# Optimization experiments

Measured on AMD Instinct MI355X. Metric: run time of the kernel, lower is better.

Reference implementation:

```python
import jax, jax.numpy as jnp
import numpy as np

N_MB = 4  # number of micro-behavior buckets; C = N_MB**2 + 1

def setup_inputs() -> dict:
    key = jax.random.key(0)
    k_q, k_k, k_b, k_w, k_a = jax.random.split(key, 5)
    b, h, S, d = 8, 8, 512, 64
    C = N_MB * N_MB + 1
    return {
        "query": jax.random.normal(k_q, (b, h, S, d), dtype=jnp.float32),
        "key": jax.random.normal(k_k, (b, h, S, d), dtype=jnp.float32),
        "b_seq": jax.random.randint(k_b, (b, S), 0, N_MB + 1, dtype=jnp.int32),
        "W1": jax.random.normal(k_w, (N_MB, h, d, d), dtype=jnp.float32) * 0.02,
        "alpha1": jax.random.normal(k_a, (C, N_MB, h), dtype=jnp.float32) * 0.02,
    }

def reference(query, key, b_seq, W1, alpha1):
    # bucket-pair index per (i, j) token pair; 0 if either token is padding
    bi = b_seq[:, :, None]  # [b, S, 1]
    bj = b_seq[:, None, :]  # [b, 1, S]
    b_mat = ((bi - 1) * N_MB + bj) * (bi * bj != 0).astype(jnp.int32)  # [b, S, S]
    # mix the n_mb base bilinear weights into C per-bucket-pair matrices
    W1_ = jnp.einsum('Bhmn,CBh->Chmn', W1, jax.nn.softmax(alpha1, axis=1))
    # full bilinear score for every bucket-pair class C (the wasteful part)
    att_all = jnp.einsum('bhim,Chmn,bhjn->bhijC', query, W1_, key)  # [b,h,S,S,C]
    # select the score matching each pair's bucket index
    idx = b_mat[:, None, :, :, None].astype(jnp.int32)  # [b,1,S,S,1] -> broadcast over h
    idx = jnp.broadcast_to(idx, att_all.shape[:4] + (1,))
    scores = jnp.take_along_axis(att_all, idx, axis=4)[..., 0]  # [b,h,S,S]
    return scores
```

## Files before the change

kernel.cpp:

```cpp
#include <hip/hip_runtime.h>
#include <stdint.h>

#define NB 4
#define NC 17
#define HH 8
#define SS 512
#define DD 64
#define CT 64

typedef __attribute__((ext_vector_type(8))) short bf16x8;
typedef __attribute__((ext_vector_type(4))) float f32x4;

#define WS_W1   0
#define WS_RIDX 1114112
#define WS_GST  (WS_RIDX + 16384)

__device__ __forceinline__ unsigned short f2bf(float f) {
  unsigned int x; __builtin_memcpy(&x, &f, 4);
  return (unsigned short)((x + 0x7fff + ((x >> 16) & 1)) >> 16);
}
__device__ __forceinline__ bf16x8 cvt8(float4 a, float4 b) {
  union { bf16x8 v; unsigned short u[8]; } t;
  t.u[0] = f2bf(a.x); t.u[1] = f2bf(a.y); t.u[2] = f2bf(a.z); t.u[3] = f2bf(a.w);
  t.u[4] = f2bf(b.x); t.u[5] = f2bf(b.y); t.u[6] = f2bf(b.z); t.u[7] = f2bf(b.w);
  return t.v;
}

__global__ __launch_bounds__(256) void k_prep(const int* __restrict__ bseq,
                                              const float* __restrict__ W1,
                                              const float* __restrict__ alpha,
                                              int* __restrict__ ridx,
                                              int* __restrict__ gst,
                                              unsigned short* __restrict__ W1mbf) {
  int tid = threadIdx.x;
  if (blockIdx.x < 8) {
    int b = blockIdx.x;
    __shared__ int cnt[5], base[6], cur[5];
    if (tid < 5) cnt[tid] = 0;
    __syncthreads();
    for (int j = tid; j < SS; j += blockDim.x) atomicAdd(&cnt[bseq[b * SS + j]], 1);
    __syncthreads();
    if (tid == 0) {
      base[0] = 0;
      for (int k = 0; k < 5; k++) base[k + 1] = base[k] + cnt[k];
      for (int k = 0; k < 6; k++) gst[b * 6 + k] = base[k];
    }
    __syncthreads();
    if (tid < 5) cur[tid] = base[tid];
    __syncthreads();
    for (int j = tid; j < SS; j += blockDim.x) {
      int p = atomicAdd(&cur[bseq[b * SS + j]], 1);
      ridx[b * SS + p] = j;
    }
  } else {
    int cb = blockIdx.x - 8;
    int c = cb >> 3, hh = cb & 7;
    __shared__ float sm[NB];
    if (tid == 0) {
      float a[NB], mx = -1e30f;
      for (int B = 0; B < NB; B++) { a[B] = alpha[(c * NB + B) * HH + hh]; mx = fmaxf(mx, a[B]); }
      float s = 0.f;
      for (int B = 0; B < NB; B++) { a[B] = __expf(a[B] - mx); s += a[B]; }
      for (int B = 0; B < NB; B++) sm[B] = a[B] / s;
    }
    __syncthreads();
    float s0 = sm[0], s1 = sm[1], s2 = sm[2], s3 = sm[3];
    for (int idx = tid; idx < DD * DD; idx += blockDim.x) {
      float v = W1[((0 * HH + hh) * DD * DD) + idx] * s0 +
                W1[((1 * HH + hh) * DD * DD) + idx] * s1 +
                W1[((2 * HH + hh) * DD * DD) + idx] * s2 +
                W1[((3 * HH + hh) * DD * DD) + idx] * s3;
      W1mbf[((size_t)(c * HH + hh)) * DD * DD + idx] = f2bf(v);
    }
  }
}

__global__ __launch_bounds__(512, 4) void k_fused(const float* __restrict__ query,
                                                  const float* __restrict__ key,
                                                  const int* __restrict__ bseq,
                                                  const unsigned short* __restrict__ W1mbf,
                                                  const int* __restrict__ ridx,
                                                  const int* __restrict__ gst,
                                                  float* __restrict__ out) {
  int bx = blockIdx.x;
  int bh = bx & 63, jt = bx >> 6;
  int b = bh >> 3, h = bh & 7;
  int j0 = jt * CT;
  int tid = threadIdx.x, wave = tid >> 6, lane = tid & 63;
  int quad = lane >> 4, l16 = lane & 15;

  __shared__ __align__(16) unsigned short Tl[5][CT][72];
  __shared__ int ord[CT], lgs[6], cnt[5], cur[5];
  __shared__ int p1list[40], p2list[40];
  __shared__ int n1s[5], n1b[5], n1tot, n2tot;

  if (tid < 5) cnt[tid] = 0;
  __syncthreads();
  int mybj = 0;
  if (tid < CT) { mybj = bseq[b * SS + j0 + tid]; atomicAdd(&cnt[mybj], 1); }
  __syncthreads();
  if (tid == 0) {
    lgs[0] = 0;
    for (int a = 0; a < 5; a++) lgs[a + 1] = lgs[a] + cnt[a];
  }
  __syncthreads();
  if (tid < 5) cur[tid] = lgs[tid];
  __syncthreads();
  if (tid < CT) ord[atomicAdd(&cur[mybj], 1)] = tid;
  if (tid < 5) n1s[tid] = ((lgs[tid + 1] - lgs[tid] + 15) >> 4) * ((tid == 0) ? 1 : 5);
  __syncthreads();
  if (tid == 0) {
    int a0 = 0;
    for (int a = 0; a < 5; a++) { n1b[a] = a0; a0 += n1s[a]; }
    n1tot = a0;
    int a1 = 0;
    for (int a = 0; a < 5; a++) a1 += (gst[b * 6 + a + 1] - gst[b * 6 + a] + 15) >> 4;
    n2tot = a1;
  }
  __syncthreads();
  if (tid < 5) {
    int a = tid;
    int ls = lgs[a], le = lgs[a + 1];
    int w = n1b[a];
    for (int t0 = ls; t0 < le; t0 += 16) {
      if (a == 0) {
        p1list[w++] = t0 | (le << 6) | (1 << 21);
      } else {
        for (int B = 0; B < 5; B++) {
          int c = (B == 0) ? 0 : (B - 1) * NB + a;
          p1list[w++] = t0 | (le << 6) | (c << 13) | (B << 18);
        }
      }
    }
    int w2 = 0;
    for (int aa = 0; aa < a; aa++) w2 += (gst[b * 6 + aa + 1] - gst[b * 6 + aa] + 15) >> 4;
    int gs = gst[b * 6 + a], ge = gst[b * 6 + a + 1];
    for (int p0 = gs; p0 < ge; p0 += 16)
      p2list[w2++] = p0 | (ge << 10) | (a << 20);
  }
  __syncthreads();

  for (int idx = wave; idx < n1tot; idx += 8) {
    int e = p1list[idx];
    int t0 = e & 63, le = (e >> 6) & 127, c = (e >> 13) & 31, B = (e >> 18) & 7;
    int bc = (e >> 21) & 1;
    const unsigned short* Wc = W1mbf + ((size_t)(c * HH + h) << 12);
    int p = t0 + l16; if (p > le - 1) p = le - 1;
    int cl = ord[p];
    const float* kp = &key[((size_t)(bh * SS + j0 + cl)) * DD + quad * 8];
    float4 ka = *(const float4*)kp, kb = *(const float4*)(kp + 4);
    float4 kc = *(const float4*)(kp + 32), kd = *(const float4*)(kp + 36);
    bf16x8 af0 = cvt8(ka, kb);
    bf16x8 af1 = cvt8(kc, kd);
    int cr[4];
#pragma unroll
    for (int reg = 0; reg < 4; reg++) {
      int pr = t0 + quad * 4 + reg;
      cr[reg] = (pr < le) ? ord[pr] : -1;
    }
#pragma unroll
    for (int nt = 0; nt < 4; nt++) {
      const unsigned short* wp = &Wc[(nt * 16 + l16) * DD + quad * 8];
      bf16x8 b0 = *(const bf16x8*)wp;
      bf16x8 b1 = *(const bf16x8*)(wp + 32);
      f32x4 acc = {0.f, 0.f, 0.f, 0.f};
      acc = __builtin_amdgcn_mfma_f32_16x16x32_bf16(af0, b0, acc, 0, 0, 0);
      acc = __builtin_amdgcn_mfma_f32_16x16x32_bf16(af1, b1, acc, 0, 0, 0);
#pragma unroll
      for (int reg = 0; reg < 4; reg++) {
        if (cr[reg] >= 0) {
          unsigned short v = f2bf(acc[reg]);
          if (bc) {
#pragma unroll
            for (int Bw = 0; Bw < 5; Bw++) Tl[Bw][cr[reg]][nt * 16 + l16] = v;
          } else {
            Tl[B][cr[reg]][nt * 16 + l16] = v;
          }
        }
      }
    }
  }
  __syncthreads();

  for (int i0 = wave * 2; i0 < n2tot; i0 += 16) {
    int e0 = p2list[i0];
    bool has1 = (i0 + 1) < n2tot;
    int e1 = has1 ? p2list[i0 + 1] : e0;

    int p0a = e0 & 1023, gea = (e0 >> 10) & 1023, Ba = e0 >> 20;
    int p0b = e1 & 1023, geb = (e1 >> 10) & 1023, Bb = e1 >> 20;

    int pa = p0a + l16; if (pa > gea - 1) pa = gea - 1;
    int pb = p0b + l16; if (pb > geb - 1) pb = geb - 1;
    int ra = ridx[b * SS + pa];
    int rb = ridx[b * SS + pb];
    const float* qa = &query[((size_t)(bh * SS + ra)) * DD + quad * 8];
    const float* qb = &query[((size_t)(bh * SS + rb)) * DD + quad * 8];
    float4 a0 = *(const float4*)qa, a1 = *(const float4*)(qa + 4);
    float4 a2 = *(const float4*)(qa + 32), a3 = *(const float4*)(qa + 36);
    float4 b0_ = *(const float4*)qb, b1_ = *(const float4*)(qb + 4);
    float4 b2_ = *(const float4*)(qb + 32), b3_ = *(const float4*)(qb + 36);
    bf16x8 afa0 = cvt8(a0, a1), afa1 = cvt8(a2, a3);
    bf16x8 afb0 = cvt8(b0_, b1_), afb1 = cvt8(b2_, b3_);

    int rra[4], rrb[4];
#pragma unroll
    for (int reg = 0; reg < 4; reg++) {
      int pra = p0a + quad * 4 + reg;
      rra[reg] = (pra < gea) ? ridx[b * SS + pra] : -1;
      int prb = p0b + quad * 4 + reg;
      rrb[reg] = (has1 && prb < geb) ? ridx[b * SS + prb] : -1;
    }
#pragma unroll
    for (int ct = 0; ct < CT / 16; ct++) {
      const unsigned short* tpa = &Tl[Ba][ct * 16 + l16][quad * 8];
      const unsigned short* tpb = &Tl[Bb][ct * 16 + l16][quad * 8];
      bf16x8 ba0 = *(const bf16x8*)tpa;
      bf16x8 ba1 = *(const bf16x8*)(tpa + 32);
      bf16x8 bb0 = *(const bf16x8*)tpb;
      bf16x8 bb1 = *(const bf16x8*)(tpb + 32);
      f32x4 acca = {0.f, 0.f, 0.f, 0.f}, accb = {0.f, 0.f, 0.f, 0.f};
      acca = __builtin_amdgcn_mfma_f32_16x16x32_bf16(afa0, ba0, acca, 0, 0, 0);
      accb = __builtin_amdgcn_mfma_f32_16x16x32_bf16(afb0, bb0, accb, 0, 0, 0);
      acca = __builtin_amdgcn_mfma_f32_16x16x32_bf16(afa1, ba1, acca, 0, 0, 0);
      accb = __builtin_amdgcn_mfma_f32_16x16x32_bf16(afb1, bb1, accb, 0, 0, 0);
#pragma unroll
      for (int reg = 0; reg < 4; reg++) {
        if (rra[reg] >= 0)
          out[((size_t)(bh * SS + rra[reg])) * SS + j0 + ct * 16 + l16] = acca[reg];
        if (rrb[reg] >= 0)
          out[((size_t)(bh * SS + rrb[reg])) * SS + j0 + ct * 16 + l16] = accb[reg];
      }
    }
  }
}

extern "C" void kernel_launch(void* const* d_in, const int* in_sizes, int n_in,
                              void* d_out, int out_size, void* d_ws, size_t ws_size,
                              hipStream_t stream) {
  const float* q = (const float*)d_in[0];
  const float* k = (const float*)d_in[1];
  const int* bseq = (const int*)d_in[2];
  const float* W1 = (const float*)d_in[3];
  const float* alpha = (const float*)d_in[4];
  float* out = (float*)d_out;
  char* ws = (char*)d_ws;
  unsigned short* W1mbf = (unsigned short*)(ws + WS_W1);
  int* ridx = (int*)(ws + WS_RIDX);
  int* gst = (int*)(ws + WS_GST);

  hipLaunchKernelGGL(k_prep, dim3(8 + NC * HH), dim3(256), 0, stream,
                     bseq, W1, alpha, ridx, gst, W1mbf);
  hipLaunchKernelGGL(k_fused, dim3(64 * (SS / CT)), dim3(512), 0, stream,
                     q, k, bseq, W1mbf, ridx, gst, out);
}
```

Before: 123.8 us.

## Use ballot-based bucketing, LDS ridx cache, 12 waves, setprio, nontemporal stores

The prep kernel now blends W1 with float4 loads and packed bf16 stores. The fused kernel replaces the multi-barrier atomic bucket sort with a single-wave ballot/popcount sort and caches the batch's ridx table in LDS. Blocks grow from 512 to 768 threads (12 waves), MFMA sections are wrapped in s_setprio, and output writes use nontemporal stores. These aim to cut sync overhead, global index loads and cache pollution from the large output, at the cost of more LDS and fewer registers per thread.

Result: faster. 119.9 us (-3.1%).

```diff
diff --git a/kernel.cpp b/kernel.cpp
--- a/kernel.cpp
+++ b/kernel.cpp
@@ -65,17 +65,27 @@
     }
     __syncthreads();
     float s0 = sm[0], s1 = sm[1], s2 = sm[2], s3 = sm[3];
-    for (int idx = tid; idx < DD * DD; idx += blockDim.x) {
-      float v = W1[((0 * HH + hh) * DD * DD) + idx] * s0 +
-                W1[((1 * HH + hh) * DD * DD) + idx] * s1 +
-                W1[((2 * HH + hh) * DD * DD) + idx] * s2 +
-                W1[((3 * HH + hh) * DD * DD) + idx] * s3;
-      W1mbf[((size_t)(c * HH + hh)) * DD * DD + idx] = f2bf(v);
-    }
-  }
-}
-
-__global__ __launch_bounds__(512, 4) void k_fused(const float* __restrict__ query,
+    const float* w0p = &W1[((0 * HH + hh) << 12)];
+    const float* w1p = &W1[((1 * HH + hh) << 12)];
+    const float* w2p = &W1[((2 * HH + hh) << 12)];
+    const float* w3p = &W1[((3 * HH + hh) << 12)];
+    unsigned short* dst = &W1mbf[((size_t)(c * HH + hh)) << 12];
+    for (int idx = tid * 4; idx < DD * DD; idx += 1024) {
+      float4 w0 = *(const float4*)(w0p + idx);
+      float4 w1 = *(const float4*)(w1p + idx);
+      float4 w2 = *(const float4*)(w2p + idx);
+      float4 w3 = *(const float4*)(w3p + idx);
+      union { unsigned short u[4]; uint2 v; } o;
+      o.u[0] = f2bf(w0.x * s0 + w1.x * s1 + w2.x * s2 + w3.x * s3);
+      o.u[1] = f2bf(w0.y * s0 + w1.y * s1 + w2.y * s2 + w3.y * s3);
+      o.u[2] = f2bf(w0.z * s0 + w1.z * s1 + w2.z * s2 + w3.z * s3);
+      o.u[3] = f2bf(w0.w * s0 + w1.w * s1 + w2.w * s2 + w3.w * s3);
+      *(uint2*)(dst + idx) = o.v;
+    }
+  }
+}
+
+__global__ __launch_bounds__(768, 6) void k_fused(const float* __restrict__ query,
                                                   const float* __restrict__ key,
                                                   const int* __restrict__ bseq,
                                                   const unsigned short* __restrict__ W1mbf,
@@ -90,57 +100,63 @@
   int quad = lane >> 4, l16 = lane & 15;
 
   __shared__ __align__(16) unsigned short Tl[5][CT][72];
-  __shared__ int ord[CT], lgs[6], cnt[5], cur[5];
+  __shared__ int ord[CT];
+  __shared__ int ridxs[SS];
   __shared__ int p1list[40], p2list[40];
-  __shared__ int n1s[5], n1b[5], n1tot, n2tot;
-
-  if (tid < 5) cnt[tid] = 0;
-  __syncthreads();
-  int mybj = 0;
-  if (tid < CT) { mybj = bseq[b * SS + j0 + tid]; atomicAdd(&cnt[mybj], 1); }
-  __syncthreads();
-  if (tid == 0) {
-    lgs[0] = 0;
-    for (int a = 0; a < 5; a++) lgs[a + 1] = lgs[a] + cnt[a];
-  }
-  __syncthreads();
-  if (tid < 5) cur[tid] = lgs[tid];
-  __syncthreads();
-  if (tid < CT) ord[atomicAdd(&cur[mybj], 1)] = tid;
-  if (tid < 5) n1s[tid] = ((lgs[tid + 1] - lgs[tid] + 15) >> 4) * ((tid == 0) ? 1 : 5);
-  __syncthreads();
-  if (tid == 0) {
-    int a0 = 0;
-    for (int a = 0; a < 5; a++) { n1b[a] = a0; a0 += n1s[a]; }
-    n1tot = a0;
-    int a1 = 0;
-    for (int a = 0; a < 5; a++) a1 += (gst[b * 6 + a + 1] - gst[b * 6 + a] + 15) >> 4;
-    n2tot = a1;
-  }
-  __syncthreads();
-  if (tid < 5) {
-    int a = tid;
-    int ls = lgs[a], le = lgs[a + 1];
-    int w = n1b[a];
-    for (int t0 = ls; t0 < le; t0 += 16) {
-      if (a == 0) {
-        p1list[w++] = t0 | (le << 6) | (1 << 21);
-      } else {
-        for (int B = 0; B < 5; B++) {
-          int c = (B == 0) ? 0 : (B - 1) * NB + a;
-          p1list[w++] = t0 | (le << 6) | (c << 13) | (B << 18);
+  __shared__ int n1tot, n2tot;
+
+  if (tid < SS) ridxs[tid] = ridx[b * SS + tid];
+
+  if (wave == 0) {
+    int mybj = bseq[b * SS + j0 + lane];
+    unsigned long long mm[5];
+    int pb[6];
+    pb[0] = 0;
+#pragma unroll
+    for (int a = 0; a < 5; a++) {
+      mm[a] = __ballot(mybj == a);
+      pb[a + 1] = pb[a] + (int)__popcll(mm[a]);
+    }
+    int pos = pb[mybj] + (int)__popcll(mm[mybj] & ((1ull << lane) - 1ull));
+    ord[pos] = lane;
+
+    int n1b_[5]; int t = 0;
+#pragma unroll
+    for (int a = 0; a < 5; a++) {
+      n1b_[a] = t;
+      t += ((pb[a + 1] - pb[a] + 15) >> 4) * ((a == 0) ? 1 : 5);
+    }
+    if (lane == 0) n1tot = t;
+
+    if (lane < 5) {
+      int a = lane;
+      int ls = pb[a], le = pb[a + 1];
+      int w = n1b_[a];
+      for (int t0 = ls; t0 < le; t0 += 16) {
+        if (a == 0) {
+          p1list[w++] = t0 | (le << 6) | (1 << 21);
+        } else {
+#pragma unroll
+          for (int B = 0; B < 5; B++) {
+            int c = (B == 0) ? 0 : (B - 1) * NB + a;
+            p1list[w++] = t0 | (le << 6) | (c << 13) | (B << 18);
+          }
         }
       }
-    }
-    int w2 = 0;
-    for (int aa = 0; aa < a; aa++) w2 += (gst[b * 6 + aa + 1] - gst[b * 6 + aa] + 15) >> 4;
-    int gs = gst[b * 6 + a], ge = gst[b * 6 + a + 1];
-    for (int p0 = gs; p0 < ge; p0 += 16)
-      p2list[w2++] = p0 | (ge << 10) | (a << 20);
+      int g[6];
+#pragma unroll
+      for (int k = 0; k < 6; k++) g[k] = gst[b * 6 + k];
+      int w2 = 0;
+      for (int aa = 0; aa < a; aa++) w2 += (g[aa + 1] - g[aa] + 15) >> 4;
+      int gs = g[a], ge = g[a + 1];
+      for (int p0 = gs; p0 < ge; p0 += 16)
+        p2list[w2++] = p0 | (ge << 10) | (a << 20);
+      if (a == 4) n2tot = w2;
+    }
   }
   __syncthreads();
 
-  for (int idx = wave; idx < n1tot; idx += 8) {
+  for (int idx = wave; idx < n1tot; idx += 12) {
     int e = p1list[idx];
     int t0 = e & 63, le = (e >> 6) & 127, c = (e >> 13) & 31, B = (e >> 18) & 7;
     int bc = (e >> 21) & 1;
@@ -164,8 +180,10 @@
       bf16x8 b0 = *(const bf16x8*)wp;
       bf16x8 b1 = *(const bf16x8*)(wp + 32);
       f32x4 acc = {0.f, 0.f, 0.f, 0.f};
+      __builtin_amdgcn_s_setprio(1);
       acc = __builtin_amdgcn_mfma_f32_16x16x32_bf16(af0, b0, acc, 0, 0, 0);
       acc = __builtin_amdgcn_mfma_f32_16x16x32_bf16(af1, b1, acc, 0, 0, 0);
+      __builtin_amdgcn_s_setprio(0);
 #pragma unroll
       for (int reg = 0; reg < 4; reg++) {
         if (cr[reg] >= 0) {
@@ -182,7 +200,7 @@
   }
   __syncthreads();
 
-  for (int i0 = wave * 2; i0 < n2tot; i0 += 16) {
+  for (int i0 = wave * 2; i0 < n2tot; i0 += 24) {
     int e0 = p2list[i0];
     bool has1 = (i0 + 1) < n2tot;
     int e1 = has1 ? p2list[i0 + 1] : e0;
@@ -191,25 +209,26 @@
     int p0b = e1 & 1023, geb = (e1 >> 10) & 1023, Bb = e1 >> 20;
 
     int pa = p0a + l16; if (pa > gea - 1) pa = gea - 1;
-    int pb = p0b + l16; if (pb > geb - 1) pb = geb - 1;
-    int ra = ridx[b * SS + pa];
-    int rb = ridx[b * SS + pb];
+    int ra = ridxs[pa];
     const float* qa = &query[((size_t)(bh * SS + ra)) * DD + quad * 8];
-    const float* qb = &query[((size_t)(bh * SS + rb)) * DD + quad * 8];
     float4 a0 = *(const float4*)qa, a1 = *(const float4*)(qa + 4);
     float4 a2 = *(const float4*)(qa + 32), a3 = *(const float4*)(qa + 36);
+    bf16x8 afa0 = cvt8(a0, a1), afa1 = cvt8(a2, a3);
+
+    int pb_ = p0b + l16; if (pb_ > geb - 1) pb_ = geb - 1;
+    int rb = ridxs[pb_];
+    const float* qb = &query[((size_t)(bh * SS + rb)) * DD + quad * 8];
     float4 b0_ = *(const float4*)qb, b1_ = *(const float4*)(qb + 4);
     float4 b2_ = *(const float4*)(qb + 32), b3_ = *(const float4*)(qb + 36);
-    bf16x8 afa0 = cvt8(a0, a1), afa1 = cvt8(a2, a3);
     bf16x8 afb0 = cvt8(b0_, b1_), afb1 = cvt8(b2_, b3_);
 
     int rra[4], rrb[4];
 #pragma unroll
     for (int reg = 0; reg < 4; reg++) {
       int pra = p0a + quad * 4 + reg;
-      rra[reg] = (pra < gea) ? ridx[b * SS + pra] : -1;
+      rra[reg] = (pra < gea) ? ridxs[pra] : -1;
       int prb = p0b + quad * 4 + reg;
-      rrb[reg] = (has1 && prb < geb) ? ridx[b * SS + prb] : -1;
+      rrb[reg] = (has1 && prb < geb) ? ridxs[prb] : -1;
     }
 #pragma unroll
     for (int ct = 0; ct < CT / 16; ct++) {
@@ -220,16 +239,20 @@
       bf16x8 bb0 = *(const bf16x8*)tpb;
       bf16x8 bb1 = *(const bf16x8*)(tpb + 32);
       f32x4 acca = {0.f, 0.f, 0.f, 0.f}, accb = {0.f, 0.f, 0.f, 0.f};
+      __builtin_amdgcn_s_setprio(1);
       acca = __builtin_amdgcn_mfma_f32_16x16x32_bf16(afa0, ba0, acca, 0, 0, 0);
       accb = __builtin_amdgcn_mfma_f32_16x16x32_bf16(afb0, bb0, accb, 0, 0, 0);
       acca = __builtin_amdgcn_mfma_f32_16x16x32_bf16(afa1, ba1, acca, 0, 0, 0);
       accb = __builtin_amdgcn_mfma_f32_16x16x32_bf16(afb1, bb1, accb, 0, 0, 0);
+      __builtin_amdgcn_s_setprio(0);
 #pragma unroll
       for (int reg = 0; reg < 4; reg++) {
         if (rra[reg] >= 0)
-          out[((size_t)(bh * SS + rra[reg])) * SS + j0 + ct * 16 + l16] = acca[reg];
+          __builtin_nontemporal_store(acca[reg],
+              &out[((size_t)(bh * SS + rra[reg])) * SS + j0 + ct * 16 + l16]);
         if (rrb[reg] >= 0)
-          out[((size_t)(bh * SS + rrb[reg])) * SS + j0 + ct * 16 + l16] = accb[reg];
+          __builtin_nontemporal_store(accb[reg],
+              &out[((size_t)(bh * SS + rrb[reg])) * SS + j0 + ct * 16 + l16]);
       }
     }
   }
@@ -251,6 +274,6 @@
 
   hipLaunchKernelGGL(k_prep, dim3(8 + NC * HH), dim3(256), 0, stream,
                      bseq, W1, alpha, ridx, gst, W1mbf);
-  hipLaunchKernelGGL(k_fused, dim3(64 * (SS / CT)), dim3(512), 0, stream,
+  hipLaunchKernelGGL(k_fused, dim3(64 * (SS / CT)), dim3(768), 0, stream,
                      q, k, bseq, W1mbf, ridx, gst, out);
 }
```
